# Kernel tuning notes

Measured on AMD Instinct MI355X. Metric: run time of the kernel, lower is better.

Reference implementation:

```python
import jax, jax.numpy as jnp
import numpy as np
from jax import lax

B, S, D, F = 2, 4096, 1024, 4096
LN_EPS = 1e-6

def _layer_norm(x, scale, bias):
    mu = jnp.mean(x, axis=-1, keepdims=True)
    var = jnp.mean(jnp.square(x - mu), axis=-1, keepdims=True)
    return (x - mu) * lax.rsqrt(var + LN_EPS) * scale + bias

def _gate_loop(q, k, v, a):
    # max-headed GateLoop: one head per channel, scalar complex state per channel
    # h_t = a_t * h_{t-1} + k_t * v_t ; y_t = q_t * h_t
    kv = (k * v).astype(jnp.complex64)
    def comb(e1, e2):
        a1, x1 = e1
        a2, x2 = e2
        return (a1 * a2, a2 * x1 + x2)
    _, h = lax.associative_scan(comb, (a, kv), axis=1)
    return q.astype(jnp.complex64) * h

def setup_inputs() -> dict:
    key = jax.random.key(0)
    ks = jax.random.split(key, 12)
    sd = 1.0 / np.sqrt(D)
    sf = 1.0 / np.sqrt(F)
    return {
        "x": jax.random.normal(ks[0], (B, S, D), jnp.float32),
        "Wq": jax.random.normal(ks[1], (D, D), jnp.float32) * sd,
        "Wk": jax.random.normal(ks[2], (D, D), jnp.float32) * sd,
        "Wv": jax.random.normal(ks[3], (D, D), jnp.float32) * sd,
        "Wa": jax.random.normal(ks[4], (D, 2 * D), jnp.float32) * sd,
        "Wg": jax.random.normal(ks[5], (D, D), jnp.float32) * sd,
        "Wo": jax.random.normal(ks[6], (D, D), jnp.float32) * sd,
        "ln1_scale": jnp.ones((D,), jnp.float32),
        "ln1_bias": jnp.zeros((D,), jnp.float32),
        "W1": jax.random.normal(ks[7], (D, F), jnp.float32) * sd,
        "b1": jax.random.normal(ks[8], (F,), jnp.float32) * 1e-6,
        "W2": jax.random.normal(ks[9], (F, D), jnp.float32) * sf,
        "b2": jax.random.normal(ks[10], (D,), jnp.float32) * 1e-6,
        "ln2_scale": jnp.ones((D,), jnp.float32),
        "ln2_bias": jnp.zeros((D,), jnp.float32),
    }

def reference(x, Wq, Wk, Wv, Wa, Wg, Wo, ln1_scale, ln1_bias, W1, b1, W2, b2, ln2_scale, ln2_bias):
    q = x @ Wq
    k = x @ Wk
    v = x @ Wv
    a = x @ Wa
    a_real, a_imag = jnp.split(a, 2, axis=-1)
    a_c = a_real + 1j * a_imag
    magnitude = jnp.abs(a_c)
    phase = jnp.angle(a_c)
    a_c = jax.nn.sigmoid(magnitude).astype(jnp.complex64) * jnp.exp(1j * phase)
    g = x.astype(jnp.complex64) @ Wg.astype(jnp.complex64)
    y = _gate_loop(q, k, v, a_c)
    y = y * (g * jax.nn.sigmoid(g))  # silu on complex g
    y = y @ Wo.astype(jnp.complex64)
    y = y.real
    # dropout deterministic (training=False)
    y = _layer_norm(y + x, ln1_scale, ln1_bias)
    h = jax.nn.gelu(y @ W1 + b1)
    out = h @ W2 + b2
    out = _layer_norm(out + y, ln2_scale, ln2_bias)
    return out
```

## Files before the change

### kernel.cpp

```cpp
#include <hip/hip_runtime.h>
#include <cstdint>

typedef unsigned short u16;
typedef unsigned int u32;

#define AS1 __attribute__((address_space(1)))
#define AS3 __attribute__((address_space(3)))

typedef _Float16 f16x8 __attribute__((ext_vector_type(8)));
typedef float f32x4 __attribute__((ext_vector_type(4)));

static constexpr int Bb = 2, Ss = 4096, Dd = 1024, Ff = 4096;
static constexpr int Mtok = Bb * Ss;
static constexpr int NCH = 256;
static constexpr int TCH = Ss / NCH;
static constexpr int PW = 6144;

__device__ __forceinline__ float h2f(u16 u) {
    union { u16 u; _Float16 h; } w; w.u = u; return (float)w.h;
}
__device__ __forceinline__ u16 f2h(float f) {
    union { _Float16 h; u16 u; } w; w.h = (_Float16)f; return w.u;
}

__device__ __forceinline__ float gelu_fast(float v) {
    float u = 1.5957691216057308f * (v + 0.044715f * v * v * v);
    return v / (1.f + __expf(-u));
}

__device__ __forceinline__ void gload_lds16(const u16* g, u16* l) {
    __builtin_amdgcn_global_load_lds((const AS1 u32*)g, (AS3 u32*)l, 16, 0, 0);
}

__global__ __launch_bounds__(256) void prep_fused(
    const float* __restrict__ x, u16* __restrict__ xb,
    const float* __restrict__ Wq, const float* __restrict__ Wk,
    const float* __restrict__ Wv, const float* __restrict__ Wa,
    const float* __restrict__ Wg, const float* __restrict__ Wo,
    const float* __restrict__ W1, const float* __restrict__ W2,
    u16* __restrict__ WTcat, u16* __restrict__ WTo,
    u16* __restrict__ WT1, u16* __restrict__ WT2) {
    __shared__ u16 t[32][33];
    const int tid = threadIdx.x;
    const int idx = blockIdx.x;
    if (idx < 8192) {
        const long i = ((long)idx * 256 + tid) * 4;
        float4 f = *(const float4*)(x + i);
        ushort4 o;
        o.x = f2h(f.x); o.y = f2h(f.y); o.z = f2h(f.z); o.w = f2h(f.w);
        *(ushort4*)(xb + i) = o;
        return;
    }
    const float* src; u16* dst; int K, N, ti;
    if (idx < 9216)       { src = Wq; dst = WTcat;             K = 1024; N = 1024; ti = idx - 8192; }
    else if (idx < 10240) { src = Wk; dst = WTcat + (1u << 20); K = 1024; N = 1024; ti = idx - 9216; }
    else if (idx < 11264) { src = Wv; dst = WTcat + (2u << 20); K = 1024; N = 1024; ti = idx - 10240; }
    else if (idx < 13312) { src = Wa; dst = WTcat + (3u << 20); K = 1024; N = 2048; ti = idx - 11264; }
    else if (idx < 14336) { src = Wg; dst = WTcat + (5u << 20); K = 1024; N = 1024; ti = idx - 13312; }
    else if (idx < 15360) { src = Wo; dst = WTo;               K = 1024; N = 1024; ti = idx - 14336; }
    else if (idx < 19456) { src = W1; dst = WT1;               K = 1024; N = 4096; ti = idx - 15360; }
    else                  { src = W2; dst = WT2;               K = 4096; N = 1024; ti = idx - 19456; }
    const int tiles_x = N >> 5;
    const int bx = ti % tiles_x, by = ti / tiles_x;
    const int n0 = bx << 5, k0 = by << 5;
    const int tx = tid & 31, ty = tid >> 5;
#pragma unroll
    for (int r = 0; r < 4; r++) {
        const int row = ty + r * 8;
        t[row][tx] = f2h(src[(long)(k0 + row) * N + n0 + tx]);
    }
    __syncthreads();
    const int cx = (tid & 15) << 1;
    const int ry = tid >> 4;
#pragma unroll
    for (int r = 0; r < 2; r++) {
        const int row = ry + r * 16;
        u32 v = (u32)t[cx][row] | ((u32)t[cx + 1][row] << 16);
        *(u32*)(dst + (long)(n0 + row) * K + k0 + cx) = v;
    }
}

template <int EPI>
__global__ __launch_bounds__(512, 2) void gemm8p(const u16* __restrict__ A,
                                                 const u16* __restrict__ BT,
                                                 u16* __restrict__ C,
                                                 const float* __restrict__ bias,
                                                 int M, int N, int K,
                                                 int lda, int ldc) {
    extern __shared__ u16 lds[];
    const int tid = threadIdx.x;

    const int ntn = N >> 8;
    const int total = (M >> 8) * ntn;
    const int tpb = total / (int)gridDim.x;
    const int cpx = total >> 3;

    const int srow = tid >> 3;
    const int scol = ((tid & 7) ^ (srow & 7)) << 3;
    const long lda64 = (long)lda << 6;
    const long ldb64 = (long)K << 6;

    const int nt = K >> 6;

    auto bases_for = [&](int t, int& tm, int& tn, const u16*& Ab, const u16*& Bb) {
        if (t > tpb - 1) t = tpb - 1;
        const int ti = (int)blockIdx.x + t * (int)gridDim.x;
        const int b = (ti & 7) * cpx + (ti >> 3);
        tm = (b / ntn) << 8;
        tn = (b % ntn) << 8;
        Ab = A + (long)(tm + srow) * lda + scol;
        Bb = BT + (long)(tn + srow) * (long)K + scol;
    };

    auto stA = [&](u16* bufbase, int h, const u16* Ab, int kt) {
        u16* d = bufbase + h * 8192 + tid * 8;
        const u16* g = Ab + (long)(h * 128) * lda + (kt << 6);
        gload_lds16(g, d);
        gload_lds16(g + lda64, d + 4096);
    };
    auto stB = [&](u16* bufbase, int h, const u16* Bb, int kt) {
        u16* d = bufbase + 16384 + h * 8192 + tid * 8;
        const u16* g = Bb + (long)(h * 128) * (long)K + (kt << 6);
        gload_lds16(g, d);
        gload_lds16(g + ldb64, d + 4096);
    };

    const int wid = tid >> 6, lane = tid & 63;
    const int r16 = lane & 15, q = lane >> 4;
    const int wm = (wid >> 2) * 128;
    const int wn = (wid & 3) * 64;
    const int r7 = r16 & 7;
    const int cx0 = (q ^ r7) << 3;
    const int cx1 = ((4 | q) ^ r7) << 3;
    const int aoff = (wm + r16) * 64;
    const int boff = 16384 + (wn + r16) * 64;

    f32x4 acc[8][4];
#pragma unroll
    for (int i = 0; i < 8; i++)
#pragma unroll
        for (int j = 0; j < 4; j++) acc[i][j] = (f32x4){0.f, 0.f, 0.f, 0.f};

    int tmc, tnc, tmn, tnn;
    const u16 *Ac, *Bc, *An, *Bn;
    bases_for(0, tmc, tnc, Ac, Bc);
    bases_for(1, tmn, tnn, An, Bn);

    stA(lds, 0, Ac, 0);
    stA(lds, 1, Ac, 0);
    stB(lds, 0, Bc, 0);
    stB(lds, 1, Bc, 0);
    stB(lds + 32768, 0, Bc, 1);
    stB(lds + 32768, 1, Bc, 1);

    for (int t = 0; t < tpb; ++t) {
        for (int it = 0; it < nt; ++it) {
            u16* sb = lds + ((it & 1) << 15);
            u16* so = lds + (((it & 1) ^ 1) << 15);

            asm volatile("s_waitcnt vmcnt(4)" ::: "memory");
            __builtin_amdgcn_s_barrier();

            f16x8 vb[4][2];
#pragma unroll
            for (int ni = 0; ni < 4; ni++) {
                vb[ni][0] = *(const f16x8*)(sb + boff + ni * 1024 + cx0);
                vb[ni][1] = *(const f16x8*)(sb + boff + ni * 1024 + cx1);
            }

#pragma unroll
            for (int p = 0; p < 4; ++p) {
                f16x8 pa[2][2];
#pragma unroll
                for (int m2 = 0; m2 < 2; m2++) {
                    pa[m2][0] = *(const f16x8*)(sb + aoff + (2 * p + m2) * 1024 + cx0);
                    pa[m2][1] = *(const f16x8*)(sb + aoff + (2 * p + m2) * 1024 + cx1);
                }
                if (p == 0) {
                    if (it + 1 < nt) stA(so, 0, Ac, it + 1);
                    else             stA(so, 0, An, 0);
                } else if (p == 1) {
                    if (it + 1 < nt) stA(so, 1, Ac, it + 1);
                    else             stA(so, 1, An, 0);
                } else if (p == 2) {
                    if (it + 2 < nt) stB(sb, 0, Bc, it + 2);
                    else             stB(sb, 0, Bn, it + 2 - nt);
                } else {
                    if (it + 2 < nt) stB(sb, 1, Bc, it + 2);
                    else             stB(sb, 1, Bn, it + 2 - nt);
                }
                __builtin_amdgcn_s_barrier();
                asm volatile("s_waitcnt lgkmcnt(0)" ::: "memory");
                __builtin_amdgcn_s_setprio(1);
#pragma unroll
                for (int m2 = 0; m2 < 2; m2++)
#pragma unroll
                    for (int ni = 0; ni < 4; ni++) {
                        acc[2 * p + m2][ni] = __builtin_amdgcn_mfma_f32_16x16x32_f16(
                            pa[m2][0], vb[ni][0], acc[2 * p + m2][ni], 0, 0, 0);
                        acc[2 * p + m2][ni] = __builtin_amdgcn_mfma_f32_16x16x32_f16(
                            pa[m2][1], vb[ni][1], acc[2 * p + m2][ni], 0, 0, 0);
                    }
                __builtin_amdgcn_s_setprio(0);
                __builtin_amdgcn_s_barrier();
            }
        }

#pragma unroll
        for (int mi = 0; mi < 8; mi++) {
#pragma unroll
            for (int ni = 0; ni < 4; ni++) {
                const int gcol = tnc + wn + ni * 16 + r16;
                float bv = 0.f;
                if (EPI) bv = bias[gcol];
#pragma unroll
                for (int j = 0; j < 4; j++) {
                    const int grow = tmc + wm + mi * 16 + q * 4 + j;
                    float v = acc[mi][ni][j];
                    if (EPI) v += bv;
                    if (EPI == 1) v = gelu_fast(v);
                    C[(long)grow * ldc + gcol] = f2h(v);
                    acc[mi][ni][j] = 0.f;
                }
            }
        }
        tmc = tmn; tnc = tnn; Ac = An; Bc = Bn;
        bases_for(t + 2, tmn, tnn, An, Bn);
    }

    asm volatile("s_waitcnt vmcnt(0)" ::: "memory");
}

template <int EPI>
__global__ __launch_bounds__(512, 2) void gemm8p_n128(const u16* __restrict__ A,
                                                      const u16* __restrict__ BT,
                                                      u16* __restrict__ C,
                                                      const float* __restrict__ bias,
                                                      int M, int N, int K,
                                                      int lda, int ldc) {
    extern __shared__ u16 lds[];
    const int tid = threadIdx.x;

    const int ntn = N >> 7;
    int bid = blockIdx.x;
    {
        const int cpx = gridDim.x >> 3;
        bid = (bid & 7) * cpx + (bid >> 3);
    }
    const int tm = (bid / ntn) << 8;
    const int tn = (bid % ntn) << 7;

    const int srow = tid >> 3;
    const int scol = ((tid & 7) ^ (srow & 7)) << 3;
    const u16* Abase = A + (long)(tm + srow) * lda + scol;
    const u16* Bbase = BT + (long)(tn + srow) * (long)K + scol;
    const long lda64 = (long)lda << 6;
    const long ldb64 = (long)K << 6;

    const int nt = K >> 6;

    auto stA = [&](u16* bufbase, int h, int kt) {
        u16* d = bufbase + h * 8192 + tid * 8;
        const u16* g = Abase + (long)(h * 128) * lda + (kt << 6);
        gload_lds16(g, d);
        gload_lds16(g + lda64, d + 4096);
    };
    auto stB = [&](u16* bufbase, int kt) {
        u16* d = bufbase + 16384 + tid * 8;
        const u16* g = Bbase + (kt << 6);
        gload_lds16(g, d);
        gload_lds16(g + ldb64, d + 4096);
    };

    const int wid = tid >> 6, lane = tid & 63;
    const int r16 = lane & 15, q = lane >> 4;
    const int wm = (wid >> 1) * 64;
    const int wn = (wid & 1) * 64;
    const int r7 = r16 & 7;
    const int cx0 = (q ^ r7) << 3;
    const int cx1 = ((4 | q) ^ r7) << 3;
    const int aoff = (wm + r16) * 64;
    const int boff = 16384 + (wn + r16) * 64;

    f32x4 acc[4][4];
#pragma unroll
    for (int i = 0; i < 4; i++)
#pragma unroll
        for (int j = 0; j < 4; j++) acc[i][j] = (f32x4){0.f, 0.f, 0.f, 0.f};

    {
        const int t1 = nt > 1 ? 1 : 0;
        stA(lds, 0, 0);
        stA(lds, 1, 0);
        stB(lds, 0);
        stB(lds + 24576, t1);
    }

    for (int it = 0; it < nt; ++it) {
        u16* sb = lds + (it & 1) * 24576;
        u16* so = lds + ((it & 1) ^ 1) * 24576;
        const int tA = (it + 1 < nt) ? it + 1 : nt - 1;
        const int tB = (it + 2 < nt) ? it + 2 : nt - 1;

        asm volatile("s_waitcnt vmcnt(2)" ::: "memory");
        __builtin_amdgcn_s_barrier();

        f16x8 vb[4][2];
#pragma unroll
        for (int ni = 0; ni < 4; ni++) {
            vb[ni][0] = *(const f16x8*)(sb + boff + ni * 1024 + cx0);
            vb[ni][1] = *(const f16x8*)(sb + boff + ni * 1024 + cx1);
        }

#pragma unroll
        for (int p = 0; p < 2; ++p) {
            f16x8 pa[2][2];
#pragma unroll
            for (int m2 = 0; m2 < 2; m2++) {
                pa[m2][0] = *(const f16x8*)(sb + aoff + (2 * p + m2) * 1024 + cx0);
                pa[m2][1] = *(const f16x8*)(sb + aoff + (2 * p + m2) * 1024 + cx1);
            }
            if (p == 0) {
                stA(so, 0, tA);
            } else {
                stA(so, 1, tA);
                stB(sb, tB);
            }
            __builtin_amdgcn_s_barrier();
            asm volatile("s_waitcnt lgkmcnt(0)" ::: "memory");
            __builtin_amdgcn_s_setprio(1);
#pragma unroll
            for (int m2 = 0; m2 < 2; m2++)
#pragma unroll
                for (int ni = 0; ni < 4; ni++) {
                    acc[2 * p + m2][ni] = __builtin_amdgcn_mfma_f32_16x16x32_f16(
                        pa[m2][0], vb[ni][0], acc[2 * p + m2][ni], 0, 0, 0);
                    acc[2 * p + m2][ni] = __builtin_amdgcn_mfma_f32_16x16x32_f16(
                        pa[m2][1], vb[ni][1], acc[2 * p + m2][ni], 0, 0, 0);
                }
            __builtin_amdgcn_s_setprio(0);
            __builtin_amdgcn_s_barrier();
        }
    }

    asm volatile("s_waitcnt vmcnt(0)" ::: "memory");

#pragma unroll
    for (int mi = 0; mi < 4; mi++) {
#pragma unroll
        for (int ni = 0; ni < 4; ni++) {
            const int gcol = tn + wn + ni * 16 + r16;
            float bv = 0.f;
            if (EPI) bv = bias[gcol];
#pragma unroll
            for (int j = 0; j < 4; j++) {
                const int grow = tm + wm + mi * 16 + q * 4 + j;
                float v = acc[mi][ni][j];
                if (EPI) v += bv;
                if (EPI == 1) v = gelu_fast(v);
                C[(long)grow * ldc + gcol] = f2h(v);
            }
        }
    }
}

__device__ __forceinline__ void a_transform(float ar, float ai, float& cr, float& ci) {
    float m = sqrtf(ar * ar + ai * ai);
    float sg = 1.f / (1.f + __expf(-m));
    float sc = sg / fmaxf(m, 1e-30f);
    cr = ar * sc;
    ci = ai * sc;
}

__global__ __launch_bounds__(256) void scan1(const u16* __restrict__ pcat,
                                             float4* __restrict__ sum4) {
    const int b = blockIdx.y, c = blockIdx.x;
    const int d0 = threadIdx.x << 2;
    float Arp[4], Aip[4], Xr[4], Xi[4];
#pragma unroll
    for (int j = 0; j < 4; j++) { Arp[j] = 1.f; Aip[j] = 0.f; Xr[j] = 0.f; Xi[j] = 0.f; }
    const long rowbase = (long)b * Ss + (long)c * TCH;
#pragma unroll 2
    for (int s = 0; s < TCH; ++s) {
        const long ro = (rowbase + s) * PW;
        ushort4 uar = *(const ushort4*)(pcat + ro + 3072 + d0);
        ushort4 uai = *(const ushort4*)(pcat + ro + 4096 + d0);
        ushort4 ukk = *(const ushort4*)(pcat + ro + 1024 + d0);
        ushort4 uvv = *(const ushort4*)(pcat + ro + 2048 + d0);
        const u16* ear = (const u16*)&uar;
        const u16* eai = (const u16*)&uai;
        const u16* ekk = (const u16*)&ukk;
        const u16* evv = (const u16*)&uvv;
#pragma unroll
        for (int j = 0; j < 4; j++) {
            float cr, ci;
            a_transform(h2f(ear[j]), h2f(eai[j]), cr, ci);
            float kv = h2f(ekk[j]) * h2f(evv[j]);
            float nXr = cr * Xr[j] - ci * Xi[j] + kv;
            float nXi = cr * Xi[j] + ci * Xr[j];
            Xr[j] = nXr; Xi[j] = nXi;
            float nAr = cr * Arp[j] - ci * Aip[j];
            float nAi = cr * Aip[j] + ci * Arp[j];
            Arp[j] = nAr; Aip[j] = nAi;
        }
    }
    const long sbase = ((long)b * NCH + c) * 1024 + d0;
#pragma unroll
    for (int j = 0; j < 4; j++)
        sum4[sbase + j] = make_float4(Arp[j], Aip[j], Xr[j], Xi[j]);
}

__global__ __launch_bounds__(256) void scan2(const float4* __restrict__ sum4,
                                             float2* __restrict__ carry) {
    const int idx = blockIdx.x * 256 + threadIdx.x;
    const int b = idx >> 10, d = idx & 1023;
    float hr = 0.f, hi = 0.f;
    for (int cb = 0; cb < NCH / 8; ++cb) {
        float4 t[8];
#pragma unroll
        for (int j = 0; j < 8; j++)
            t[j] = sum4[((long)b * NCH + cb * 8 + j) * 1024 + d];
#pragma unroll
        for (int j = 0; j < 8; j++) {
            carry[((long)b * NCH + cb * 8 + j) * 1024 + d] = make_float2(hr, hi);
            float nr = t[j].x * hr - t[j].y * hi + t[j].z;
            float ni = t[j].x * hi + t[j].y * hr + t[j].w;
            hr = nr; hi = ni;
        }
    }
}

__global__ __launch_bounds__(256) void scan3(u16* pcat,
                                             const float2* __restrict__ carry) {
    const int b = blockIdx.y, c = blockIdx.x;
    const int d0 = threadIdx.x << 2;
    float hr[4], hi[4];
    const long cbase = ((long)b * NCH + c) * 1024 + d0;
#pragma unroll
    for (int j = 0; j < 4; j++) {
        float2 h0 = carry[cbase + j];
        hr[j] = h0.x; hi[j] = h0.y;
    }
    const long rowbase = (long)b * Ss + (long)c * TCH;
#pragma unroll 2
    for (int s = 0; s < TCH; ++s) {
        const long ro = (rowbase + s) * PW;
        ushort4 uar = *(const ushort4*)(pcat + ro + 3072 + d0);
        ushort4 uai = *(const ushort4*)(pcat + ro + 4096 + d0);
        ushort4 ukk = *(const ushort4*)(pcat + ro + 1024 + d0);
        ushort4 uvv = *(const ushort4*)(pcat + ro + 2048 + d0);
        ushort4 ugg = *(const ushort4*)(pcat + ro + 5120 + d0);
        ushort4 uqq = *(const ushort4*)(pcat + ro + d0);
        const u16* ear = (const u16*)&uar;
        const u16* eai = (const u16*)&uai;
        const u16* ekk = (const u16*)&ukk;
        const u16* evv = (const u16*)&uvv;
        const u16* egg = (const u16*)&ugg;
        const u16* eqq = (const u16*)&uqq;
        ushort4 oy;
        u16* ey = (u16*)&oy;
#pragma unroll
        for (int j = 0; j < 4; j++) {
            float cr, ci;
            a_transform(h2f(ear[j]), h2f(eai[j]), cr, ci);
            float kv = h2f(ekk[j]) * h2f(evv[j]);
            float nhr = cr * hr[j] - ci * hi[j] + kv;
            float nhi = cr * hi[j] + ci * hr[j];
            hr[j] = nhr; hi[j] = nhi;
            float gg = h2f(egg[j]);
            float si = gg / (1.f + __expf(-gg));
            ey[j] = f2h(h2f(eqq[j]) * nhr * si);
        }
        *(ushort4*)(pcat + ro + d0) = oy;
    }
}

template <int RESF32, int OUTF32>
__global__ __launch_bounds__(256) void ln_kernel(const u16* __restrict__ a, int sa,
                                                 const void* __restrict__ bres, int sres,
                                                 const float* __restrict__ scale,
                                                 const float* __restrict__ bias,
                                                 void* __restrict__ out, int sout) {
    const int row = blockIdx.x;
    const int tid = threadIdx.x;
    const long abase = (long)row * sa;
    const long rbase = (long)row * sres;
    const long obase = (long)row * sout;
    const int d0 = tid * 4;
    float v[4];
    ushort4 ua = *(const ushort4*)(a + abase + d0);
    const u16* ea = (const u16*)&ua;
    if (RESF32) {
        float4 rf = *(const float4*)((const float*)bres + rbase + d0);
        v[0] = h2f(ea[0]) + rf.x; v[1] = h2f(ea[1]) + rf.y;
        v[2] = h2f(ea[2]) + rf.z; v[3] = h2f(ea[3]) + rf.w;
    } else {
        ushort4 ur = *(const ushort4*)((const u16*)bres + rbase + d0);
        const u16* er = (const u16*)&ur;
#pragma unroll
        for (int j = 0; j < 4; j++) v[j] = h2f(ea[j]) + h2f(er[j]);
    }
    float s = v[0] + v[1] + v[2] + v[3];
    float s2 = v[0] * v[0] + v[1] * v[1] + v[2] * v[2] + v[3] * v[3];
#pragma unroll
    for (int off = 32; off; off >>= 1) {
        s += __shfl_down(s, off);
        s2 += __shfl_down(s2, off);
    }
    __shared__ float red[8];
    const int w = tid >> 6, lane = tid & 63;
    if (lane == 0) { red[w] = s; red[4 + w] = s2; }
    __syncthreads();
    if (tid == 0) {
        float ts = red[0] + red[1] + red[2] + red[3];
        float ts2 = red[4] + red[5] + red[6] + red[7];
        float mu = ts * (1.f / 1024.f);
        float var = ts2 * (1.f / 1024.f) - mu * mu;
        red[0] = mu;
        red[1] = rsqrtf(var + 1e-6f);
    }
    __syncthreads();
    const float mu = red[0], rs = red[1];
    float4 sc = *(const float4*)(scale + d0);
    float4 bi = *(const float4*)(bias + d0);
    float y0 = (v[0] - mu) * rs * sc.x + bi.x;
    float y1 = (v[1] - mu) * rs * sc.y + bi.y;
    float y2 = (v[2] - mu) * rs * sc.z + bi.z;
    float y3 = (v[3] - mu) * rs * sc.w + bi.w;
    if (OUTF32) {
        *(float4*)((float*)out + obase + d0) = make_float4(y0, y1, y2, y3);
    } else {
        ushort4 o;
        o.x = f2h(y0); o.y = f2h(y1); o.z = f2h(y2); o.w = f2h(y3);
        *(ushort4*)((u16*)out + obase + d0) = o;
    }
}

extern "C" void kernel_launch(void* const* d_in, const int* in_sizes, int n_in,
                              void* d_out, int out_size, void* d_ws, size_t ws_size,
                              hipStream_t stream) {
    const float* x    = (const float*)d_in[0];
    const float* Wq   = (const float*)d_in[1];
    const float* Wk   = (const float*)d_in[2];
    const float* Wv   = (const float*)d_in[3];
    const float* Wa   = (const float*)d_in[4];
    const float* Wg   = (const float*)d_in[5];
    const float* Wo   = (const float*)d_in[6];
    const float* ln1s = (const float*)d_in[7];
    const float* ln1b = (const float*)d_in[8];
    const float* W1   = (const float*)d_in[9];
    const float* b1   = (const float*)d_in[10];
    const float* W2   = (const float*)d_in[11];
    const float* b2   = (const float*)d_in[12];
    const float* ln2s = (const float*)d_in[13];
    const float* ln2b = (const float*)d_in[14];

    u16* ws    = (u16*)d_ws;
    u16* xb    = ws;
    u16* WTcat = xb + (8u << 20);
    u16* WTo   = WTcat + (6u << 20);
    u16* WT1   = WTo + (1u << 20);
    u16* WT2   = WT1 + (4u << 20);
    u16* pcat  = WT2 + (4u << 20);

    float4* sum4  = (float4*)WTcat;
    float2* carry = (float2*)(WTcat + (4u << 20));

    static bool attr_done = false;
    if (!attr_done) {
        hipFuncSetAttribute(reinterpret_cast<const void*>(&gemm8p<0>),
                            hipFuncAttributeMaxDynamicSharedMemorySize, 131072);
        hipFuncSetAttribute(reinterpret_cast<const void*>(&gemm8p<1>),
                            hipFuncAttributeMaxDynamicSharedMemorySize, 131072);
        hipFuncSetAttribute(reinterpret_cast<const void*>(&gemm8p_n128<0>),
                            hipFuncAttributeMaxDynamicSharedMemorySize, 98304);
        hipFuncSetAttribute(reinterpret_cast<const void*>(&gemm8p_n128<2>),
                            hipFuncAttributeMaxDynamicSharedMemorySize, 98304);
        attr_done = true;
    }


    prep_fused<<<dim3(23552), dim3(256), 0, stream>>>(x, xb, Wq, Wk, Wv, Wa, Wg, Wo,
                                                      W1, W2, WTcat, WTo, WT1, WT2);

    gemm8p<0><<<dim3(256), dim3(512), 131072, stream>>>(xb, WTcat, pcat, nullptr,
                                                        Mtok, PW, 1024, 1024, PW);
    scan1<<<dim3(NCH, Bb), dim3(256), 0, stream>>>(pcat, sum4);
    scan2<<<dim3(8), dim3(256), 0, stream>>>(sum4, carry);
    scan3<<<dim3(NCH, Bb), dim3(256), 0, stream>>>(pcat, carry);
    gemm8p_n128<0><<<dim3(256), dim3(512), 98304, stream>>>(pcat, WTo, pcat + 1024,
                                                            nullptr,
                                                            Mtok, 1024, 1024, PW, PW);
    ln_kernel<1, 0><<<dim3(Mtok), dim3(256), 0, stream>>>(pcat + 1024, PW, x, 1024,
                                                          ln1s, ln1b, pcat, PW);
    gemm8p<1><<<dim3(256), dim3(512), 131072, stream>>>(pcat, WT1, pcat + 2048, b1,
                                                        Mtok, Ff, 1024, PW, PW);
    gemm8p_n128<2><<<dim3(256), dim3(512), 98304, stream>>>(pcat + 2048, WT2,
                                                            pcat + 1024, b2,
                                                            Mtok, 1024, Ff, PW, PW);
    ln_kernel<0, 1><<<dim3(Mtok), dim3(256), 0, stream>>>(pcat + 1024, PW, pcat, PW,
                                                          ln2s, ln2b, d_out, 1024);
}
```

Measured before the change: 547.8 us.

## Merge GEMM inner phases into two halves and halve scan chunk count

The 8-wave GEMM main loop goes from four sub-phases per K-tile (each loading two A fragments, issuing one LDS prefetch and running 16 MFMAs between barriers) to two phases, each loading four A fragments, issuing two prefetch stores and running 32 MFMAs. This halves the number of barriers per K-step and gives longer MFMA bursts, at the cost of more live A-fragment registers. Separately, the scan chunk count drops from 256 to 128 (longer chunks, fewer carries), and the carry buffer offset moves because the chunk-sum array shrinks.

```diff
diff --git a/kernel.cpp b/kernel.cpp
--- a/kernel.cpp
+++ b/kernel.cpp
@@ -12,7 +12,7 @@
 
 static constexpr int Bb = 2, Ss = 4096, Dd = 1024, Ff = 4096;
 static constexpr int Mtok = Bb * Ss;
-static constexpr int NCH = 256;
+static constexpr int NCH = 128;
 static constexpr int TCH = Ss / NCH;
 static constexpr int PW = 6144;
 
@@ -167,43 +167,60 @@
                 vb[ni][0] = *(const f16x8*)(sb + boff + ni * 1024 + cx0);
                 vb[ni][1] = *(const f16x8*)(sb + boff + ni * 1024 + cx1);
             }
-
-#pragma unroll
-            for (int p = 0; p < 4; ++p) {
-                f16x8 pa[2][2];
-#pragma unroll
-                for (int m2 = 0; m2 < 2; m2++) {
-                    pa[m2][0] = *(const f16x8*)(sb + aoff + (2 * p + m2) * 1024 + cx0);
-                    pa[m2][1] = *(const f16x8*)(sb + aoff + (2 * p + m2) * 1024 + cx1);
+            f16x8 pa[4][2];
+#pragma unroll
+            for (int m = 0; m < 4; m++) {
+                pa[m][0] = *(const f16x8*)(sb + aoff + m * 1024 + cx0);
+                pa[m][1] = *(const f16x8*)(sb + aoff + m * 1024 + cx1);
+            }
+            if (it + 1 < nt) {
+                stA(so, 0, Ac, it + 1);
+                stA(so, 1, Ac, it + 1);
+            } else {
+                stA(so, 0, An, 0);
+                stA(so, 1, An, 0);
+            }
+            __builtin_amdgcn_s_barrier();
+            asm volatile("s_waitcnt lgkmcnt(0)" ::: "memory");
+            __builtin_amdgcn_s_setprio(1);
+#pragma unroll
+            for (int m = 0; m < 4; m++)
+#pragma unroll
+                for (int ni = 0; ni < 4; ni++) {
+                    acc[m][ni] = __builtin_amdgcn_mfma_f32_16x16x32_f16(
+                        pa[m][0], vb[ni][0], acc[m][ni], 0, 0, 0);
+                    acc[m][ni] = __builtin_amdgcn_mfma_f32_16x16x32_f16(
+                        pa[m][1], vb[ni][1], acc[m][ni], 0, 0, 0);
                 }
-                if (p == 0) {
-                    if (it + 1 < nt) stA(so, 0, Ac, it + 1);
-                    else             stA(so, 0, An, 0);
-                } else if (p == 1) {
-                    if (it + 1 < nt) stA(so, 1, Ac, it + 1);
-                    else             stA(so, 1, An, 0);
-                } else if (p == 2) {
-                    if (it + 2 < nt) stB(sb, 0, Bc, it + 2);
-                    else             stB(sb, 0, Bn, it + 2 - nt);
-                } else {
-                    if (it + 2 < nt) stB(sb, 1, Bc, it + 2);
-                    else             stB(sb, 1, Bn, it + 2 - nt);
+            __builtin_amdgcn_s_setprio(0);
+            __builtin_amdgcn_s_barrier();
+
+#pragma unroll
+            for (int m = 0; m < 4; m++) {
+                pa[m][0] = *(const f16x8*)(sb + aoff + (4 + m) * 1024 + cx0);
+                pa[m][1] = *(const f16x8*)(sb + aoff + (4 + m) * 1024 + cx1);
+            }
+            if (it + 2 < nt) {
+                stB(sb, 0, Bc, it + 2);
+                stB(sb, 1, Bc, it + 2);
+            } else {
+                stB(sb, 0, Bn, it + 2 - nt);
+                stB(sb, 1, Bn, it + 2 - nt);
+            }
+            __builtin_amdgcn_s_barrier();
+            asm volatile("s_waitcnt lgkmcnt(0)" ::: "memory");
+            __builtin_amdgcn_s_setprio(1);
+#pragma unroll
+            for (int m = 0; m < 4; m++)
+#pragma unroll
+                for (int ni = 0; ni < 4; ni++) {
+                    acc[4 + m][ni] = __builtin_amdgcn_mfma_f32_16x16x32_f16(
+                        pa[m][0], vb[ni][0], acc[4 + m][ni], 0, 0, 0);
+                    acc[4 + m][ni] = __builtin_amdgcn_mfma_f32_16x16x32_f16(
+                        pa[m][1], vb[ni][1], acc[4 + m][ni], 0, 0, 0);
                 }
-                __builtin_amdgcn_s_barrier();
-                asm volatile("s_waitcnt lgkmcnt(0)" ::: "memory");
-                __builtin_amdgcn_s_setprio(1);
-#pragma unroll
-                for (int m2 = 0; m2 < 2; m2++)
-#pragma unroll
-                    for (int ni = 0; ni < 4; ni++) {
-                        acc[2 * p + m2][ni] = __builtin_amdgcn_mfma_f32_16x16x32_f16(
-                            pa[m2][0], vb[ni][0], acc[2 * p + m2][ni], 0, 0, 0);
-                        acc[2 * p + m2][ni] = __builtin_amdgcn_mfma_f32_16x16x32_f16(
-                            pa[m2][1], vb[ni][1], acc[2 * p + m2][ni], 0, 0, 0);
-                    }
-                __builtin_amdgcn_s_setprio(0);
-                __builtin_amdgcn_s_barrier();
-            }
+            __builtin_amdgcn_s_setprio(0);
+            __builtin_amdgcn_s_barrier();
         }
 
 #pragma unroll
@@ -564,7 +581,7 @@
     u16* pcat  = WT2 + (4u << 20);
 
     float4* sum4  = (float4*)WTcat;
-    float2* carry = (float2*)(WTcat + (4u << 20));
+    float2* carry = (float2*)(WTcat + (2u << 20));
 
     static bool attr_done = false;
     if (!attr_done) {
```

Measured after the change: 513.4 us. -6.3%, faster.

## Use dense per-stage buffers instead of strided pcat slices and halve scan chunks

Applied to the files above, without the earlier changes.

Intermediates (scan output, Wo output, LN1 output, FFN hidden, FFN output) now go to separate densely packed buffers with their natural row strides instead of interleaved slices of the 6144-wide pcat array. This is meant to make the downstream GEMM and layer-norm accesses contiguous and more cache friendly. The scan chunk count is also halved, so each chunk walks twice as many timesteps while scan2 has a shorter sequential carry chain. The reused buffers (xb for the scan output and LN1 output, the WTcat region for sum/carry) rely on their earlier contents no longer being needed when they are overwritten.

```diff
diff --git a/kernel.cpp b/kernel.cpp
--- a/kernel.cpp
+++ b/kernel.cpp
@@ -12,7 +12,7 @@
 
 static constexpr int Bb = 2, Ss = 4096, Dd = 1024, Ff = 4096;
 static constexpr int Mtok = Bb * Ss;
-static constexpr int NCH = 256;
+static constexpr int NCH = 128;
 static constexpr int TCH = Ss / NCH;
 static constexpr int PW = 6144;
 
@@ -430,8 +430,9 @@
     }
 }
 
-__global__ __launch_bounds__(256) void scan3(u16* pcat,
-                                             const float2* __restrict__ carry) {
+__global__ __launch_bounds__(256) void scan3(const u16* __restrict__ pcat,
+                                             const float2* __restrict__ carry,
+                                             u16* __restrict__ ybuf) {
     const int b = blockIdx.y, c = blockIdx.x;
     const int d0 = threadIdx.x << 2;
     float hr[4], hi[4];
@@ -444,7 +445,8 @@
     const long rowbase = (long)b * Ss + (long)c * TCH;
 #pragma unroll 2
     for (int s = 0; s < TCH; ++s) {
-        const long ro = (rowbase + s) * PW;
+        const long row = rowbase + s;
+        const long ro = row * PW;
         ushort4 uar = *(const ushort4*)(pcat + ro + 3072 + d0);
         ushort4 uai = *(const ushort4*)(pcat + ro + 4096 + d0);
         ushort4 ukk = *(const ushort4*)(pcat + ro + 1024 + d0);
@@ -471,7 +473,7 @@
             float si = gg / (1.f + __expf(-gg));
             ey[j] = f2h(h2f(eqq[j]) * nhr * si);
         }
-        *(ushort4*)(pcat + ro + d0) = oy;
+        *(ushort4*)(ybuf + row * 1024 + d0) = oy;
     }
 }
 
@@ -564,7 +566,13 @@
     u16* pcat  = WT2 + (4u << 20);
 
     float4* sum4  = (float4*)WTcat;
-    float2* carry = (float2*)(WTcat + (4u << 20));
+    float2* carry = (float2*)(WTcat + (2u << 20));
+
+    u16* o1   = pcat;
+    u16* hmat = pcat + (8u << 20);
+    u16* o2   = pcat + (40u << 20);
+    u16* ybuf = xb;
+    u16* yln  = xb;
 
     static bool attr_done = false;
     if (!attr_done) {
@@ -579,7 +587,6 @@
         attr_done = true;
     }
 
-
     prep_fused<<<dim3(23552), dim3(256), 0, stream>>>(x, xb, Wq, Wk, Wv, Wa, Wg, Wo,
                                                       W1, W2, WTcat, WTo, WT1, WT2);
 
@@ -587,17 +594,15 @@
                                                         Mtok, PW, 1024, 1024, PW);
     scan1<<<dim3(NCH, Bb), dim3(256), 0, stream>>>(pcat, sum4);
     scan2<<<dim3(8), dim3(256), 0, stream>>>(sum4, carry);
-    scan3<<<dim3(NCH, Bb), dim3(256), 0, stream>>>(pcat, carry);
-    gemm8p_n128<0><<<dim3(256), dim3(512), 98304, stream>>>(pcat, WTo, pcat + 1024,
-                                                            nullptr,
-                                                            Mtok, 1024, 1024, PW, PW);
-    ln_kernel<1, 0><<<dim3(Mtok), dim3(256), 0, stream>>>(pcat + 1024, PW, x, 1024,
-                                                          ln1s, ln1b, pcat, PW);
-    gemm8p<1><<<dim3(256), dim3(512), 131072, stream>>>(pcat, WT1, pcat + 2048, b1,
-                                                        Mtok, Ff, 1024, PW, PW);
-    gemm8p_n128<2><<<dim3(256), dim3(512), 98304, stream>>>(pcat + 2048, WT2,
-                                                            pcat + 1024, b2,
-                                                            Mtok, 1024, Ff, PW, PW);
-    ln_kernel<0, 1><<<dim3(Mtok), dim3(256), 0, stream>>>(pcat + 1024, PW, pcat, PW,
+    scan3<<<dim3(NCH, Bb), dim3(256), 0, stream>>>(pcat, carry, ybuf);
+    gemm8p_n128<0><<<dim3(256), dim3(512), 98304, stream>>>(ybuf, WTo, o1, nullptr,
+                                                            Mtok, 1024, 1024, 1024, 1024);
+    ln_kernel<1, 0><<<dim3(Mtok), dim3(256), 0, stream>>>(o1, 1024, x, 1024,
+                                                          ln1s, ln1b, yln, 1024);
+    gemm8p<1><<<dim3(256), dim3(512), 131072, stream>>>(yln, WT1, hmat, b1,
+                                                        Mtok, Ff, 1024, 1024, Ff);
+    gemm8p_n128<2><<<dim3(256), dim3(512), 98304, stream>>>(hmat, WT2, o2, b2,
+                                                            Mtok, 1024, Ff, Ff, 1024);
+    ln_kernel<0, 1><<<dim3(Mtok), dim3(256), 0, stream>>>(o2, 1024, yln, 1024,
                                                           ln2s, ln2b, d_out, 1024);
 }
```

Result: no change. 553.1 us (+1.0%).
